# Kernel tuning notes

Measured on AMD Instinct MI355X. Metric: run time of the kernel, lower is better.

## Reference

```python
import jax, jax.numpy as jnp
import numpy as np

N_NODES = 50000
N_EDGES = 200000
D = 128          # in_channels == num_hidden_channels == out_channels (set_out_input_dim_equal)
H = 4            # num_att_heads
C = D            # out_channels per head
R = 8            # num_relations
NEG_SLOPE = 0.2  # GATv2 leaky_relu slope


def gelu(x):
    # torch nn.GELU default = exact erf form
    return jax.nn.gelu(x, approximate=False)


def setup_inputs() -> dict:
    key = jax.random.key(0)
    ks = jax.random.split(key, 8)
    embs = jax.random.normal(ks[0], (N_NODES, D), dtype=jnp.float32)
    edge_index = jax.random.randint(ks[1], (2, N_EDGES), 0, N_NODES)
    edge_type = jax.random.randint(ks[2], (N_EDGES,), 0, R)
    # glorot for relation matrices [R, 2D, D]
    lim = float(np.sqrt(6.0 / (2 * D + D)))
    rel_matrices = jax.random.uniform(ks[3], (R, 2 * D, D), jnp.float32, -lim, lim)
    # GATv2Conv lin_l (== lin_r, share_weights=True): D -> H*C, with bias
    lim_l = float(np.sqrt(6.0 / (D + H * C)))
    W_l = jax.random.uniform(ks[4], (D, H * C), jnp.float32, -lim_l, lim_l)
    b_l = jnp.zeros((H * C,), jnp.float32)
    # lin_edge: edge_dim=D -> H*C, no bias
    W_e = jax.random.uniform(ks[5], (D, H * C), jnp.float32, -lim_l, lim_l)
    # attention vector att: [H, C]
    lim_a = float(np.sqrt(6.0 / C))
    att = jax.random.uniform(ks[6], (H, C), jnp.float32, -lim_a, lim_a)
    # final bias (concat=True -> size H*C)
    bias = jnp.zeros((H * C,), jnp.float32)
    return {"embs": embs, "edge_index": edge_index, "edge_type": edge_type,
            "rel_matrices": rel_matrices, "W_l": W_l, "b_l": b_l,
            "W_e": W_e, "att": att, "bias": bias, "batch_size": 1024}


def reference(embs, edge_index, edge_type, rel_matrices, W_l, b_l, W_e, att, bias, batch_size):
    src = edge_index[0]  # x_j / message source
    trg = edge_index[1]  # x_i / aggregation target

    # ---- create_edge_attrs: per-edge relation-specific bmm + GELU ----
    e_emb = jnp.concatenate([embs[src], embs[trg]], axis=1)  # [E, 2D]
    acc = jnp.zeros((e_emb.shape[0], D), e_emb.dtype)
    for r in range(R):  # fixed small relation set; avoids [E,2D,D] materialization
        acc = acc + jnp.where((edge_type == r)[:, None], e_emb @ rel_matrices[r], 0.0)
    edge_attr = gelu(acc)  # [E, D]

    # ---- GATv2Conv (share_weights=True, add_self_loops=False, concat) ----
    x = (embs @ W_l + b_l).reshape(N_NODES, H, C)  # lin_l == lin_r
    x_j = x[src]                                    # [E, H, C]
    x_i = x[trg]                                    # [E, H, C]
    e_p = (edge_attr @ W_e).reshape(-1, H, C)       # [E, H, C]

    z = jax.nn.leaky_relu(x_i + x_j + e_p, NEG_SLOPE)
    logits = jnp.einsum('ehc,hc->eh', z, att)       # [E, H]

    # edge softmax over incoming edges per target node (numerically stable)
    m = jax.ops.segment_max(logits, trg, num_segments=N_NODES)
    m = jnp.where(jnp.isfinite(m), m, 0.0)
    ex = jnp.exp(logits - m[trg])
    s = jax.ops.segment_sum(ex, trg, num_segments=N_NODES)
    alpha = ex / jnp.maximum(s[trg], 1e-16)         # [E, H]

    out = jax.ops.segment_sum(x_j * alpha[..., None], trg, num_segments=N_NODES)
    out = out.reshape(N_NODES, H * C) + bias        # concat heads
    # single (last) layer: no trailing dropout / GELU
    return out
```

## Files before the change

### kernel.cpp

```cpp
#include <hip/hip_runtime.h>
#include <math.h>

#define D_DIM 128
#define TWO_D 256
#define HC    512
#define NH    4
#define RNUM  8
#define BM    128

#define M_CNT  0
#define M_OFF  8
#define M_BLK  17
#define M_CUR  26
#define M_CUR2 34

typedef __attribute__((ext_vector_type(8))) short v8s;
typedef __attribute__((ext_vector_type(4))) float v4f;
typedef __attribute__((ext_vector_type(8))) unsigned short us8;

#define MFMA(a,b,c) __builtin_amdgcn_mfma_f32_16x16x32_bf16((a),(b),(c),0,0,0)

__device__ __forceinline__ float bf2f(unsigned short v){
    return __uint_as_float(((unsigned)v) << 16);
}
__device__ __forceinline__ unsigned short f2bf(float f){
    unsigned u = __float_as_uint(f);
    u += 0x7fffu + ((u >> 16) & 1u);
    return (unsigned short)(u >> 16);
}

__device__ __forceinline__ v8s frag_ld(const unsigned short* buf, int r, int chunk){
    return *(const v8s*)(buf + r * 64 + ((chunk ^ (r & 7)) << 3));
}

template<typename RowFn>
__device__ __forceinline__ void stage_gl(unsigned short* lds, RowFn rowp, int col0, int tid){
    const int lane = tid & 63;
    const int w = tid >> 6;
    #pragma unroll
    for (int i = 0; i < 4; i++){
        const int k = w * 4 + i;
        const int o = k * 1024 + lane * 16;
        const int rr = o >> 7;
        const int cp = (o & 127) >> 4;
        const int cg = cp ^ (rr & 7);
        const unsigned short* src = rowp(rr) + col0 + cg * 8;
        unsigned short* dst = lds + k * 512;
        __builtin_amdgcn_global_load_lds((const __attribute__((address_space(1))) void*)src,
                                         (__attribute__((address_space(3))) void*)dst,
                                         16, 0, 0);
    }
}

__global__ void k_prep(const float* __restrict__ embs, const float* __restrict__ rel,
                       const float* __restrict__ W_e, const float* __restrict__ W_l,
                       unsigned short* __restrict__ embs_bf, unsigned short* __restrict__ rel_t,
                       unsigned short* __restrict__ W_e_t, unsigned short* __restrict__ W_l_t,
                       int* __restrict__ meta, int* __restrict__ tcnt, int* __restrict__ tcur,
                       int N){
    const long T0 = (long)N * D_DIM;
    const long T1 = T0 + (long)RNUM * D_DIM * TWO_D;
    const long T2 = T1 + (long)HC * D_DIM;
    const long T3 = T2 + (long)HC * D_DIM;
    const long stride = (long)gridDim.x * blockDim.x;
    const long gid = (long)blockIdx.x * blockDim.x + threadIdx.x;

    for (long i = gid; i < N; i += stride){ tcnt[i] = 0; tcur[i] = 0; }
    if (gid < RNUM) meta[M_CNT + gid] = 0;

    const long NE8 = T0 / 8;
    for (long i = gid; i < NE8; i += stride){
        const float4* p = (const float4*)(embs + i * 8);
        float4 a = p[0], b = p[1];
        us8 o;
        o[0]=f2bf(a.x); o[1]=f2bf(a.y); o[2]=f2bf(a.z); o[3]=f2bf(a.w);
        o[4]=f2bf(b.x); o[5]=f2bf(b.y); o[6]=f2bf(b.z); o[7]=f2bf(b.w);
        *(us8*)(embs_bf + i * 8) = o;
    }
    for (long i = T0 + gid; i < T3; i += stride){
        if (i < T1){
            long j = i - T0;
            int r = (int)(j >> 15);
            int rem = (int)(j & 32767);
            int n = rem >> 8, k = rem & 255;
            rel_t[j] = f2bf(rel[(long)r * 32768 + (long)k * D_DIM + n]);
        } else if (i < T2){
            long j = i - T1;
            int n = (int)(j >> 7), k = (int)(j & 127);
            W_e_t[j] = f2bf(W_e[(long)k * HC + n]);
        } else {
            long j = i - T2;
            int n = (int)(j >> 7), k = (int)(j & 127);
            W_l_t[j] = f2bf(W_l[(long)k * HC + n]);
        }
    }
}

__global__ void k_count(const int* __restrict__ etype, const int* __restrict__ trg,
                        int* __restrict__ meta, int* __restrict__ tcnt, int E){
    __shared__ int h[RNUM];
    int tid = threadIdx.x;
    if (tid < RNUM) h[tid] = 0;
    __syncthreads();
    int e = blockIdx.x * 256 + tid;
    if (e < E){
        atomicAdd(&h[etype[e]], 1);
        atomicAdd(&tcnt[trg[e]], 1);
    }
    __syncthreads();
    if (tid < RNUM) atomicAdd(&meta[M_CNT + tid], h[tid]);
}

__global__ __launch_bounds__(1024) void k_tscan(const int* __restrict__ tcnt,
                                                int* __restrict__ rowptr,
                                                int* __restrict__ meta, int N){
    __shared__ int part[1024];
    const int T = 1024;
    int tid = threadIdx.x;
    if (tid == 0){
        int offv = 0, blkv = 0;
        meta[M_OFF] = 0; meta[M_BLK] = 0;
        for (int r2 = 0; r2 < RNUM; r2++){
            int c = meta[M_CNT + r2];
            offv += c; blkv += (c + BM - 1) / BM;
            meta[M_OFF + r2 + 1] = offv;
            meta[M_BLK + r2 + 1] = blkv;
            meta[M_CUR + r2] = 0;
            meta[M_CUR2 + r2] = 0;
        }
    }
    int chunk = (N + T - 1) / T;
    int lo = tid * chunk, hi = min(lo + chunk, N);
    int s = 0;
    for (int i = lo; i < hi; i++) s += tcnt[i];
    part[tid] = s;
    __syncthreads();
    for (int off = 1; off < T; off <<= 1){
        int v = (tid >= off) ? part[tid - off] : 0;
        __syncthreads();
        part[tid] += v;
        __syncthreads();
    }
    int run = (tid == 0) ? 0 : part[tid - 1];
    for (int i = lo; i < hi; i++){ rowptr[i] = run; run += tcnt[i]; }
    if (tid == T - 1) rowptr[N] = part[T - 1];
}

__global__ void k_scatter2(const int* __restrict__ etype, const int* __restrict__ trg,
                           const int* __restrict__ src,
                           const int* __restrict__ rowptr, int* __restrict__ tcur,
                           int* __restrict__ srcp, int* __restrict__ trgp,
                           int* __restrict__ etypep, int E){
    int e = blockIdx.x * 256 + threadIdx.x;
    if (e < E){
        int t = trg[e];
        int pos = rowptr[t] + atomicAdd(&tcur[t], 1);
        srcp[pos] = src[e];
        trgp[pos] = t;
        etypep[pos] = etype[e];
    }
}

__global__ void k_rscatter(const int* __restrict__ etypep, int* __restrict__ meta,
                           int* __restrict__ perm, int E){
    __shared__ int lcnt[RNUM], lbase[RNUM];
    int tid = threadIdx.x;
    if (tid < RNUM) lcnt[tid] = 0;
    __syncthreads();
    int p = blockIdx.x * 256 + tid;
    int r = 0, rank = 0;
    if (p < E){ r = etypep[p]; rank = atomicAdd(&lcnt[r], 1); }
    __syncthreads();
    if (tid < RNUM) lbase[tid] = atomicAdd(&meta[M_CUR2 + tid], lcnt[tid]);
    __syncthreads();
    if (p < E) perm[meta[M_OFF + r] + lbase[r] + rank] = p;
}

#define ZP 132

__global__ __launch_bounds__(256, 4) void k_x_mfma(
    const unsigned short* __restrict__ embs_bf, const unsigned short* __restrict__ W_l_t,
    const float* __restrict__ b_l, unsigned short* __restrict__ x_bf, int N)
{
    __shared__ __align__(16) char smem[64 * ZP * 4];
    unsigned short* Ab = (unsigned short*)smem;
    unsigned short* Bb = (unsigned short*)(smem + 16384);
    float* zb = (float*)smem;

    const int tid = threadIdx.x;
    const int n0 = blockIdx.x * BM;
    const int cg = blockIdx.y;
    const int cnt = min(BM, N - n0);
    const int w = tid >> 6, lane = tid & 63, m = lane & 15, q = lane >> 4;

    v4f acc[2][8];
    #pragma unroll
    for (int i = 0; i < 2; i++)
        #pragma unroll
        for (int j = 0; j < 8; j++) acc[i][j] = 0.f;

    #pragma unroll
    for (int ch = 0; ch < 2; ch++){
        __syncthreads();
        stage_gl(Ab, [&](int rr){ return embs_bf + (long)min(n0 + rr, N - 1) * D_DIM; },
                 ch * 64, tid);
        stage_gl(Bb, [&](int rr){ return W_l_t + (long)(cg * BM + rr) * D_DIM; },
                 ch * 64, tid);
        __syncthreads();
        #pragma unroll
        for (int ks = 0; ks < 2; ks++){
            v8s af[2], bf[8];
            #pragma unroll
            for (int rt = 0; rt < 2; rt++) af[rt] = frag_ld(Ab, w*32 + rt*16 + m, ks*4 + q);
            #pragma unroll
            for (int ct = 0; ct < 8; ct++) bf[ct] = frag_ld(Bb, ct*16 + m, ks*4 + q);
            #pragma unroll
            for (int rt = 0; rt < 2; rt++)
                #pragma unroll
                for (int ct = 0; ct < 8; ct++)
                    acc[rt][ct] = MFMA(af[rt], bf[ct], acc[rt][ct]);
        }
    }
    __syncthreads();

    for (int pp = 0; pp < 2; pp++){
        if ((w >> 1) == pp){
            int wr = (w & 1) * 32;
            #pragma unroll
            for (int rt = 0; rt < 2; rt++)
                #pragma unroll
                for (int ct = 0; ct < 8; ct++)
                    #pragma unroll
                    for (int g = 0; g < 4; g++)
                        zb[(wr + rt*16 + q*4 + g) * ZP + ct*16 + m] = acc[rt][ct][g];
        }
        __syncthreads();
        int rl = tid >> 2, pq = tid & 3;
        int row = pp * 64 + rl;
        if (row < cnt){
            const float* zp = zb + rl * ZP + pq * 32;
            const float* blp = b_l + cg * BM + pq * 32;
            long dst = (long)(n0 + row) * HC + cg * BM + pq * 32;
            #pragma unroll
            for (int g2 = 0; g2 < 4; g2++){
                us8 o;
                #pragma unroll
                for (int j = 0; j < 8; j++)
                    o[j] = f2bf(zp[g2*8 + j] + blp[g2*8 + j]);
                *(us8*)&x_bf[dst + g2*8] = o;
            }
        }
        __syncthreads();
    }
}

__global__ __launch_bounds__(256, 4) void k_attr_mfma(
    const unsigned short* __restrict__ embs_bf, const int* __restrict__ srcp,
    const int* __restrict__ trgp, const unsigned short* __restrict__ rel_t,
    const int* __restrict__ perm, const int* __restrict__ meta,
    unsigned short* __restrict__ edge_attrp)
{
    __shared__ __align__(16) char smem[64 * ZP * 4];
    unsigned short* Ab = (unsigned short*)smem;
    unsigned short* Bb = (unsigned short*)(smem + 16384);
    float* zb = (float*)smem;
    __shared__ int s_ep[BM], s_s[BM], s_t[BM];
    __shared__ int s_meta[3];

    const int tid = threadIdx.x;
    const int b = blockIdx.x;
    if (tid == 0){
        int nblk = meta[M_BLK + RNUM];
        if (b >= nblk){ s_meta[0] = -1; }
        else {
            int r = 0;
            while (b >= meta[M_BLK + r + 1]) r++;
            int chunk = b - meta[M_BLK + r];
            int base = meta[M_OFF + r] + chunk * BM;
            s_meta[0] = r; s_meta[1] = base;
            s_meta[2] = min(BM, meta[M_OFF + r + 1] - base);
        }
    }
    __syncthreads();
    const int r = s_meta[0];
    if (r < 0) return;
    const int base = s_meta[1], cnt = s_meta[2];
    if (tid < BM){
        int pos = perm[base + min(tid, cnt - 1)];
        s_ep[tid] = pos; s_s[tid] = srcp[pos]; s_t[tid] = trgp[pos];
    }
    const int w = tid >> 6, lane = tid & 63, m = lane & 15, q = lane >> 4;

    v4f acc[2][8];
    #pragma unroll
    for (int i = 0; i < 2; i++)
        #pragma unroll
        for (int j = 0; j < 8; j++) acc[i][j] = 0.f;

    __syncthreads();

    #pragma unroll
    for (int ch = 0; ch < 4; ch++){
        __syncthreads();
        stage_gl(Ab, [&](int rr){ int node = (ch < 2) ? s_s[rr] : s_t[rr];
                                  return embs_bf + (long)node * D_DIM; },
                 (ch & 1) * 64, tid);
        stage_gl(Bb, [&](int rr){ return rel_t + ((long)r * BM + rr) * TWO_D; },
                 ch * 64, tid);
        __syncthreads();
        #pragma unroll
        for (int ks = 0; ks < 2; ks++){
            v8s af[2], bf[8];
            #pragma unroll
            for (int rt = 0; rt < 2; rt++) af[rt] = frag_ld(Ab, w*32 + rt*16 + m, ks*4 + q);
            #pragma unroll
            for (int ct = 0; ct < 8; ct++) bf[ct] = frag_ld(Bb, ct*16 + m, ks*4 + q);
            #pragma unroll
            for (int rt = 0; rt < 2; rt++)
                #pragma unroll
                for (int ct = 0; ct < 8; ct++)
                    acc[rt][ct] = MFMA(af[rt], bf[ct], acc[rt][ct]);
        }
    }
    __syncthreads();

    for (int pp = 0; pp < 2; pp++){
        if ((w >> 1) == pp){
            int wr = (w & 1) * 32;
            #pragma unroll
            for (int rt = 0; rt < 2; rt++)
                #pragma unroll
                for (int ct = 0; ct < 8; ct++)
                    #pragma unroll
                    for (int g = 0; g < 4; g++)
                        zb[(wr + rt*16 + q*4 + g) * ZP + ct*16 + m] = acc[rt][ct][g];
        }
        __syncthreads();
        int rl = tid >> 2, pq = tid & 3;
        int row = pp * 64 + rl;
        if (row < cnt){
            const float* zp = zb + rl * ZP + pq * 32;
            long dst = (long)s_ep[row] * D_DIM + pq * 32;
            #pragma unroll
            for (int g2 = 0; g2 < 4; g2++){
                us8 o;
                #pragma unroll
                for (int j = 0; j < 8; j++){
                    float v = zp[g2*8 + j];
                    v = 0.5f * v * (1.f + erff(v * 0.70710678118654752f));
                    o[j] = f2bf(v);
                }
                *(us8*)&edge_attrp[dst + g2*8] = o;
            }
        }
        __syncthreads();
    }
}

__global__ __launch_bounds__(256, 4) void k_logits_mfma(
    const unsigned short* __restrict__ edge_attrp, const unsigned short* __restrict__ W_e_t,
    const float* __restrict__ att, const unsigned short* __restrict__ x_bf,
    const int* __restrict__ srcp, const int* __restrict__ trgp,
    float* __restrict__ logitsp, int E)
{
    __shared__ __align__(16) char smem[64 * ZP * 4];
    unsigned short* Ab = (unsigned short*)smem;
    unsigned short* Bb = (unsigned short*)(smem + 16384);
    float* zb = (float*)smem;
    __shared__ int s_s[BM], s_t[BM];

    const int tid = threadIdx.x;
    const int bid = blockIdx.x;
    const int g = bid >> 5, r5 = bid & 31;
    const int tile = g * 8 + (r5 & 7);
    const int h = r5 >> 3;
    const int lbv = (E + BM - 1) / BM;
    if (tile >= lbv) return;
    const int e0 = tile * BM;
    const int cnt = min(BM, E - e0);
    if (tid < BM){
        int e = e0 + min(tid, cnt - 1);
        s_s[tid] = srcp[e]; s_t[tid] = trgp[e];
    }
    const int w = tid >> 6, lane = tid & 63, m = lane & 15, q = lane >> 4;

    v4f acc[2][8];
    #pragma unroll
    for (int i = 0; i < 2; i++)
        #pragma unroll
        for (int j = 0; j < 8; j++) acc[i][j] = 0.f;

    #pragma unroll
    for (int ch = 0; ch < 2; ch++){
        __syncthreads();
        stage_gl(Ab, [&](int rr){ return edge_attrp + (long)(e0 + min(rr, cnt - 1)) * D_DIM; },
                 ch * 64, tid);
        stage_gl(Bb, [&](int rr){ return W_e_t + (long)(h * BM + rr) * D_DIM; },
                 ch * 64, tid);
        __syncthreads();
        #pragma unroll
        for (int ks = 0; ks < 2; ks++){
            v8s af[2], bf[8];
            #pragma unroll
            for (int rt = 0; rt < 2; rt++) af[rt] = frag_ld(Ab, w*32 + rt*16 + m, ks*4 + q);
            #pragma unroll
            for (int ct = 0; ct < 8; ct++) bf[ct] = frag_ld(Bb, ct*16 + m, ks*4 + q);
            #pragma unroll
            for (int rt = 0; rt < 2; rt++)
                #pragma unroll
                for (int ct = 0; ct < 8; ct++)
                    acc[rt][ct] = MFMA(af[rt], bf[ct], acc[rt][ct]);
        }
    }
    __syncthreads();

    for (int pp = 0; pp < 2; pp++){
        if ((w >> 1) == pp){
            int wr = (w & 1) * 32;
            #pragma unroll
            for (int rt = 0; rt < 2; rt++)
                #pragma unroll
                for (int ct = 0; ct < 8; ct++)
                    #pragma unroll
                    for (int g2 = 0; g2 < 4; g2++)
                        zb[(wr + rt*16 + q*4 + g2) * ZP + ct*16 + m] = acc[rt][ct][g2];
        }
        __syncthreads();
        int rl = tid >> 2, pq = tid & 3;
        int row = pp * 64 + rl;
        float part = 0.f;
        if (row < cnt){
            int s = s_s[row], t = s_t[row];
            const float* zp = zb + rl * ZP + pq * 32;
            const unsigned short* xip = x_bf + (long)t * HC + h * BM + pq * 32;
            const unsigned short* xjp = x_bf + (long)s * HC + h * BM + pq * 32;
            const float* ap = att + h * BM + pq * 32;
            #pragma unroll
            for (int g2 = 0; g2 < 4; g2++){
                us8 xi = *(const us8*)(xip + g2*8);
                us8 xj = *(const us8*)(xjp + g2*8);
                #pragma unroll
                for (int j = 0; j < 8; j++){
                    float z = zp[g2*8 + j] + bf2f(xi[j]) + bf2f(xj[j]);
                    z = (z > 0.f) ? z : 0.2f * z;
                    part += z * ap[g2*8 + j];
                }
            }
        }
        part += __shfl_xor(part, 1, 64);
        part += __shfl_xor(part, 2, 64);
        if ((tid & 3) == 0 && row < cnt)
            logitsp[(long)(e0 + row) * NH + h] = part;
        __syncthreads();
    }
}

__global__ __launch_bounds__(256) void k_agg_csr(
    const float* __restrict__ logitsp, const int* __restrict__ rowptr,
    const int* __restrict__ srcp,
    const unsigned short* __restrict__ x_bf, const float* __restrict__ bias,
    float* __restrict__ out, int N)
{
    int t = blockIdx.x * 4 + (threadIdx.x >> 6);
    if (t >= N) return;
    int lane = threadIdx.x & 63;
    int c0 = lane * 8;
    int h = lane >> 4;
    int lo = rowptr[t], hi = rowptr[t + 1];

    float acc[8];
    #pragma unroll
    for (int j = 0; j < 8; j++) acc[j] = 0.f;

    if (lo < hi){
        float mx = -3.0e38f;
        for (int i = lo; i < hi; i++)
            mx = fmaxf(mx, logitsp[(long)i * NH + h]);
        float ssum = 0.f;
        for (int i = lo; i < hi; i++){
            float ew = expf(logitsp[(long)i * NH + h] - mx);
            ssum += ew;
            us8 xv = *(const us8*)&x_bf[(long)srcp[i] * HC + c0];
            #pragma unroll
            for (int j = 0; j < 8; j++) acc[j] += ew * bf2f(xv[j]);
        }
        float inv = 1.f / fmaxf(ssum, 1e-16f);
        #pragma unroll
        for (int j = 0; j < 8; j++) acc[j] *= inv;
    }
    long dst = (long)t * HC + c0;
    *(float4*)&out[dst]     = make_float4(acc[0] + bias[c0+0], acc[1] + bias[c0+1],
                                          acc[2] + bias[c0+2], acc[3] + bias[c0+3]);
    *(float4*)&out[dst + 4] = make_float4(acc[4] + bias[c0+4], acc[5] + bias[c0+5],
                                          acc[6] + bias[c0+6], acc[7] + bias[c0+7]);
}

extern "C" void kernel_launch(void* const* d_in, const int* in_sizes, int n_in,
                              void* d_out, int out_size, void* d_ws, size_t ws_size,
                              hipStream_t stream) {
    const float* embs       = (const float*)d_in[0];
    const int*   edge_index = (const int*)  d_in[1];
    const int*   etype      = (const int*)  d_in[2];
    const float* rel        = (const float*)d_in[3];
    const float* W_l        = (const float*)d_in[4];
    const float* b_l        = (const float*)d_in[5];
    const float* W_e        = (const float*)d_in[6];
    const float* att        = (const float*)d_in[7];
    const float* bias       = (const float*)d_in[8];

    const int N = in_sizes[0] / D_DIM;
    const int E = in_sizes[1] / 2;
    const int* src = edge_index;
    const int* trg = edge_index + E;

    char* ws = (char*)d_ws;
    size_t off = 0;
    unsigned short* x_bf = (unsigned short*)(ws + off);      off += (size_t)N * HC * 2;
    unsigned short* embs_bf = (unsigned short*)(ws + off);   off += (size_t)N * D_DIM * 2;
    unsigned short* edge_attrp = (unsigned short*)(ws + off); off += (size_t)E * D_DIM * 2;
    unsigned short* rel_t = (unsigned short*)(ws + off);     off += (size_t)RNUM * D_DIM * TWO_D * 2;
    unsigned short* W_e_t = (unsigned short*)(ws + off);     off += (size_t)HC * D_DIM * 2;
    unsigned short* W_l_t = (unsigned short*)(ws + off);     off += (size_t)HC * D_DIM * 2;
    float* logitsp = (float*)(ws + off);                     off += (size_t)E * NH * 4;
    int* perm = (int*)(ws + off);                            off += (size_t)E * 4;
    int* meta = (int*)(ws + off);                            off += 64 * 4;
    int* tcnt = (int*)(ws + off);                            off += (size_t)N * 4;
    int* tcur = (int*)(ws + off);                            off += (size_t)N * 4;
    int* rowptr = (int*)(ws + off);                          off += (size_t)(N + 1) * 4;
    int* etypep = (int*)(ws + off);                          off += (size_t)E * 4;
    int* srcp = (int*)(ws + off);                            off += (size_t)E * 4;
    int* trgp = (int*)(ws + off);                            off += (size_t)E * 4;

    float* out = (float*)d_out;

    const int eb = (E + 255) / 256;
    const int ab = (E + BM - 1) / BM + RNUM;
    const int lb = (E + BM - 1) / BM;
    const int lgrid = ((lb + 7) / 8) * 32;

    k_prep<<<2048, 256, 0, stream>>>(embs, rel, W_e, W_l, embs_bf, rel_t, W_e_t, W_l_t,
                                     meta, tcnt, tcur, N);
    k_count<<<eb, 256, 0, stream>>>(etype, trg, meta, tcnt, E);
    k_tscan<<<1, 1024, 0, stream>>>(tcnt, rowptr, meta, N);
    k_scatter2<<<eb, 256, 0, stream>>>(etype, trg, src, rowptr, tcur, srcp, trgp, etypep, E);
    k_rscatter<<<eb, 256, 0, stream>>>(etypep, meta, perm, E);
    k_x_mfma<<<dim3((N + BM - 1) / BM, NH), 256, 0, stream>>>(embs_bf, W_l_t, b_l, x_bf, N);
    k_attr_mfma<<<ab, 256, 0, stream>>>(embs_bf, srcp, trgp, rel_t, perm, meta, edge_attrp);
    k_logits_mfma<<<lgrid, 256, 0, stream>>>(edge_attrp, W_e_t, att, x_bf, srcp, trgp,
                                             logitsp, E);
    k_agg_csr<<<(N + 3) / 4, 256, 0, stream>>>(logitsp, rowptr, srcp, x_bf, bias, out, N);
}
```

Before: 462.0 us.

## Fuse target scan into node GEMM kernel and read weight fragments from global

The single-block target-count scan is folded into the node projection GEMM as an extra block, removing one launch and letting the serial scan overlap with the GEMM work. All three MFMA GEMM kernels stop staging the weight tile into LDS and instead load B fragments directly from global memory, relying on L2 caching of the small weight matrices. This cuts LDS traffic and a sync-bound staging step, but it adds uncoalesced strided global loads in the inner loop. The scan now uses 256 threads instead of 1024, which makes its serial chunks longer.

After: 621.6 us. 34.5% more time.

```diff
diff --git a/kernel.cpp b/kernel.cpp
--- a/kernel.cpp
+++ b/kernel.cpp
@@ -31,6 +31,9 @@
 
 __device__ __forceinline__ v8s frag_ld(const unsigned short* buf, int r, int chunk){
     return *(const v8s*)(buf + r * 64 + ((chunk ^ (r & 7)) << 3));
+}
+__device__ __forceinline__ v8s frag_gl(const unsigned short* gbase, long row, long stride, int k0){
+    return *(const v8s*)(gbase + row * stride + k0);
 }
 
 template<typename RowFn>
@@ -111,41 +114,6 @@
     if (tid < RNUM) atomicAdd(&meta[M_CNT + tid], h[tid]);
 }
 
-__global__ __launch_bounds__(1024) void k_tscan(const int* __restrict__ tcnt,
-                                                int* __restrict__ rowptr,
-                                                int* __restrict__ meta, int N){
-    __shared__ int part[1024];
-    const int T = 1024;
-    int tid = threadIdx.x;
-    if (tid == 0){
-        int offv = 0, blkv = 0;
-        meta[M_OFF] = 0; meta[M_BLK] = 0;
-        for (int r2 = 0; r2 < RNUM; r2++){
-            int c = meta[M_CNT + r2];
-            offv += c; blkv += (c + BM - 1) / BM;
-            meta[M_OFF + r2 + 1] = offv;
-            meta[M_BLK + r2 + 1] = blkv;
-            meta[M_CUR + r2] = 0;
-            meta[M_CUR2 + r2] = 0;
-        }
-    }
-    int chunk = (N + T - 1) / T;
-    int lo = tid * chunk, hi = min(lo + chunk, N);
-    int s = 0;
-    for (int i = lo; i < hi; i++) s += tcnt[i];
-    part[tid] = s;
-    __syncthreads();
-    for (int off = 1; off < T; off <<= 1){
-        int v = (tid >= off) ? part[tid - off] : 0;
-        __syncthreads();
-        part[tid] += v;
-        __syncthreads();
-    }
-    int run = (tid == 0) ? 0 : part[tid - 1];
-    for (int i = lo; i < hi; i++){ rowptr[i] = run; run += tcnt[i]; }
-    if (tid == T - 1) rowptr[N] = part[T - 1];
-}
-
 __global__ void k_scatter2(const int* __restrict__ etype, const int* __restrict__ trg,
                            const int* __restrict__ src,
                            const int* __restrict__ rowptr, int* __restrict__ tcur,
@@ -178,18 +146,55 @@
 
 #define ZP 132
 
-__global__ __launch_bounds__(256, 4) void k_x_mfma(
+__global__ __launch_bounds__(256, 4) void k_x_tscan(
     const unsigned short* __restrict__ embs_bf, const unsigned short* __restrict__ W_l_t,
-    const float* __restrict__ b_l, unsigned short* __restrict__ x_bf, int N)
+    const float* __restrict__ b_l, unsigned short* __restrict__ x_bf, int N,
+    const int* __restrict__ tcnt, int* __restrict__ rowptr, int* __restrict__ meta)
 {
     __shared__ __align__(16) char smem[64 * ZP * 4];
+
+    if (blockIdx.x == gridDim.x - 1){
+        int* part = (int*)smem;
+        const int T = 256;
+        int tid = threadIdx.x;
+        if (tid == 0){
+            int offv = 0, blkv = 0;
+            meta[M_OFF] = 0; meta[M_BLK] = 0;
+            for (int r2 = 0; r2 < RNUM; r2++){
+                int c = meta[M_CNT + r2];
+                offv += c; blkv += (c + BM - 1) / BM;
+                meta[M_OFF + r2 + 1] = offv;
+                meta[M_BLK + r2 + 1] = blkv;
+                meta[M_CUR + r2] = 0;
+                meta[M_CUR2 + r2] = 0;
+            }
+        }
+        int chunk = (N + T - 1) / T;
+        int lo = tid * chunk, hi = min(lo + chunk, N);
+        int s = 0;
+        for (int i = lo; i < hi; i++) s += tcnt[i];
+        part[tid] = s;
+        __syncthreads();
+        for (int off = 1; off < T; off <<= 1){
+            int v = (tid >= off) ? part[tid - off] : 0;
+            __syncthreads();
+            part[tid] += v;
+            __syncthreads();
+        }
+        int run = (tid == 0) ? 0 : part[tid - 1];
+        for (int i = lo; i < hi; i++){ rowptr[i] = run; run += tcnt[i]; }
+        if (tid == T - 1) rowptr[N] = part[T - 1];
+        return;
+    }
+
     unsigned short* Ab = (unsigned short*)smem;
-    unsigned short* Bb = (unsigned short*)(smem + 16384);
     float* zb = (float*)smem;
 
+    const int xb = (N + BM - 1) / BM;
+    const int bid = blockIdx.x;
+    const int cg = bid / xb;
+    const int n0 = (bid - cg * xb) * BM;
     const int tid = threadIdx.x;
-    const int n0 = blockIdx.x * BM;
-    const int cg = blockIdx.y;
     const int cnt = min(BM, N - n0);
     const int w = tid >> 6, lane = tid & 63, m = lane & 15, q = lane >> 4;
 
@@ -204,16 +209,16 @@
         __syncthreads();
         stage_gl(Ab, [&](int rr){ return embs_bf + (long)min(n0 + rr, N - 1) * D_DIM; },
                  ch * 64, tid);
-        stage_gl(Bb, [&](int rr){ return W_l_t + (long)(cg * BM + rr) * D_DIM; },
-                 ch * 64, tid);
         __syncthreads();
         #pragma unroll
         for (int ks = 0; ks < 2; ks++){
+            const int k0 = ch * 64 + (ks * 4 + q) * 8;
             v8s af[2], bf[8];
             #pragma unroll
             for (int rt = 0; rt < 2; rt++) af[rt] = frag_ld(Ab, w*32 + rt*16 + m, ks*4 + q);
             #pragma unroll
-            for (int ct = 0; ct < 8; ct++) bf[ct] = frag_ld(Bb, ct*16 + m, ks*4 + q);
+            for (int ct = 0; ct < 8; ct++)
+                bf[ct] = frag_gl(W_l_t, (long)(cg * BM + ct*16 + m), D_DIM, k0);
             #pragma unroll
             for (int rt = 0; rt < 2; rt++)
                 #pragma unroll
@@ -262,7 +267,6 @@
 {
     __shared__ __align__(16) char smem[64 * ZP * 4];
     unsigned short* Ab = (unsigned short*)smem;
-    unsigned short* Bb = (unsigned short*)(smem + 16384);
     float* zb = (float*)smem;
     __shared__ int s_ep[BM], s_s[BM], s_t[BM];
     __shared__ int s_meta[3];
@@ -305,16 +309,16 @@
         stage_gl(Ab, [&](int rr){ int node = (ch < 2) ? s_s[rr] : s_t[rr];
                                   return embs_bf + (long)node * D_DIM; },
                  (ch & 1) * 64, tid);
-        stage_gl(Bb, [&](int rr){ return rel_t + ((long)r * BM + rr) * TWO_D; },
-                 ch * 64, tid);
         __syncthreads();
         #pragma unroll
         for (int ks = 0; ks < 2; ks++){
+            const int k0 = ch * 64 + (ks * 4 + q) * 8;
             v8s af[2], bf[8];
             #pragma unroll
             for (int rt = 0; rt < 2; rt++) af[rt] = frag_ld(Ab, w*32 + rt*16 + m, ks*4 + q);
             #pragma unroll
-            for (int ct = 0; ct < 8; ct++) bf[ct] = frag_ld(Bb, ct*16 + m, ks*4 + q);
+            for (int ct = 0; ct < 8; ct++)
+                bf[ct] = frag_gl(rel_t, (long)r * BM + ct*16 + m, TWO_D, k0);
             #pragma unroll
             for (int rt = 0; rt < 2; rt++)
                 #pragma unroll
@@ -365,7 +369,6 @@
 {
     __shared__ __align__(16) char smem[64 * ZP * 4];
     unsigned short* Ab = (unsigned short*)smem;
-    unsigned short* Bb = (unsigned short*)(smem + 16384);
     float* zb = (float*)smem;
     __shared__ int s_s[BM], s_t[BM];
 
@@ -395,16 +398,16 @@
         __syncthreads();
         stage_gl(Ab, [&](int rr){ return edge_attrp + (long)(e0 + min(rr, cnt - 1)) * D_DIM; },
                  ch * 64, tid);
-        stage_gl(Bb, [&](int rr){ return W_e_t + (long)(h * BM + rr) * D_DIM; },
-                 ch * 64, tid);
         __syncthreads();
         #pragma unroll
         for (int ks = 0; ks < 2; ks++){
+            const int k0 = ch * 64 + (ks * 4 + q) * 8;
             v8s af[2], bf[8];
             #pragma unroll
             for (int rt = 0; rt < 2; rt++) af[rt] = frag_ld(Ab, w*32 + rt*16 + m, ks*4 + q);
             #pragma unroll
-            for (int ct = 0; ct < 8; ct++) bf[ct] = frag_ld(Bb, ct*16 + m, ks*4 + q);
+            for (int ct = 0; ct < 8; ct++)
+                bf[ct] = frag_gl(W_e_t, (long)(h * BM + ct*16 + m), D_DIM, k0);
             #pragma unroll
             for (int rt = 0; rt < 2; rt++)
                 #pragma unroll
@@ -536,15 +539,16 @@
     const int eb = (E + 255) / 256;
     const int ab = (E + BM - 1) / BM + RNUM;
     const int lb = (E + BM - 1) / BM;
+    const int xb = (N + BM - 1) / BM;
     const int lgrid = ((lb + 7) / 8) * 32;
 
     k_prep<<<2048, 256, 0, stream>>>(embs, rel, W_e, W_l, embs_bf, rel_t, W_e_t, W_l_t,
                                      meta, tcnt, tcur, N);
     k_count<<<eb, 256, 0, stream>>>(etype, trg, meta, tcnt, E);
-    k_tscan<<<1, 1024, 0, stream>>>(tcnt, rowptr, meta, N);
+    k_x_tscan<<<xb * NH + 1, 256, 0, stream>>>(embs_bf, W_l_t, b_l, x_bf, N,
+                                               tcnt, rowptr, meta);
     k_scatter2<<<eb, 256, 0, stream>>>(etype, trg, src, rowptr, tcur, srcp, trgp, etypep, E);
     k_rscatter<<<eb, 256, 0, stream>>>(etypep, meta, perm, E);
-    k_x_mfma<<<dim3((N + BM - 1) / BM, NH), 256, 0, stream>>>(embs_bf, W_l_t, b_l, x_bf, N);
     k_attr_mfma<<<ab, 256, 0, stream>>>(embs_bf, srcp, trgp, rel_t, perm, meta, edge_attrp);
     k_logits_mfma<<<lgrid, 256, 0, stream>>>(edge_attrp, W_e_t, att, x_bf, srcp, trgp,
                                              logitsp, E);
```
